# Optimization experiments

Hardware: AMD Instinct MI355X
Metric: run time of the kernel (lower is better)

## Reference

```python
import jax, jax.numpy as jnp
import numpy as np

N_NODES = 100000
N_EDGES = 1000000
D_IN = 64
D_OUT = 64


def setup_inputs() -> dict:
    key = jax.random.key(0)
    k_x, k_e, k_wl, k_bl, k_wr = jax.random.split(key, 5)
    x = jax.random.normal(k_x, (N_NODES, D_IN), dtype=jnp.float32)
    edge_index = jax.random.randint(k_e, (2, N_EDGES), 0, N_NODES, dtype=jnp.int64)
    scale = 1.0 / np.sqrt(D_IN)
    # SAGEConv params: lin_l (neighbor path, with bias), lin_r (root/self path, no bias)
    W_l = jax.random.uniform(k_wl, (D_OUT, D_IN), dtype=jnp.float32, minval=-scale, maxval=scale)
    b_l = jax.random.uniform(k_bl, (D_OUT,), dtype=jnp.float32, minval=-scale, maxval=scale)
    W_r = jax.random.uniform(k_wr, (D_OUT, D_IN), dtype=jnp.float32, minval=-scale, maxval=scale)
    return {"x": x, "edge_index": edge_index, "W_l": W_l, "b_l": b_l, "W_r": W_r}


def reference(x, edge_index, W_l, b_l, W_r):
    # PyG SAGEConv with mean aggregation:
    #   out = lin_l(mean_{j in N(i)} x_j) + lin_r(x_i);  then ReLU (from GCN.forward)
    src = edge_index[0]  # message sources
    dst = edge_index[1]  # aggregation targets
    n = x.shape[0]
    msg = x[src]  # [E, D_IN] gather
    agg = jax.ops.segment_sum(msg, dst, num_segments=n)  # [N, D_IN]
    deg = jax.ops.segment_sum(jnp.ones((src.shape[0],), x.dtype), dst, num_segments=n)
    mean = agg / jnp.maximum(deg, 1.0)[:, None]  # isolated nodes -> 0
    out = mean @ W_l.T + b_l + x @ W_r.T
    return jax.nn.relu(out)
```

## Files before the change

kernel.cpp:

```cpp
#include <hip/hip_runtime.h>

#define N_NODES 100000
#define N_EDGES 1000000
#define D 64

#define NFINE 782
#define CAP2 1536
#define CHUNK 2048
#define EDGE_BLOCKS 489
#define CONV_BLOCKS 6250
#define CONS_BLOCKS 3128
#define STR 132
#define SCAP 512

typedef unsigned short u16;
typedef unsigned int u32;
using bf16x8 = __attribute__((ext_vector_type(8))) short;
using f32x4  = __attribute__((ext_vector_type(4))) float;

__device__ __forceinline__ u16 f2bf(float f) {
    u32 u = __float_as_uint(f);
    return (u16)((u + 0x7FFF + ((u >> 16) & 1)) >> 16);
}
__device__ __forceinline__ float bf2f(u16 v) {
    return __uint_as_float(((u32)v) << 16);
}

__global__ __launch_bounds__(256) void conv_zero_kernel(
    const float* __restrict__ x, u16* __restrict__ xb,
    int* __restrict__ cur2) {
    if (blockIdx.x == CONV_BLOCKS) {
        for (int j = threadIdx.x; j < NFINE; j += 256) cur2[j] = 0;
        return;
    }
    int i = blockIdx.x * 256 + threadIdx.x;
    float4 v = ((const float4*)x)[i];
    ((ushort4*)xb)[i] = make_ushort4(f2bf(v.x), f2bf(v.y), f2bf(v.z), f2bf(v.w));
}

__global__ __launch_bounds__(1024) void build4_kernel(
    const int* __restrict__ ei, int* __restrict__ cur2,
    u32* __restrict__ pairs2) {
    __shared__ u32 sorted[CHUNK];
    __shared__ u16 binof[CHUNK];
    __shared__ int hist[NFINE];
    __shared__ int off_l[NFINE];
    __shared__ int cur_l[NFINE];
    __shared__ int base_g[NFINE];
    __shared__ int wsum[16];

    int b = blockIdx.x;
    int t = threadIdx.x;
    int ln = t & 63;
    int wv = t >> 6;

    const u32* uu = (const u32*)ei;
    int f = 1;
    #pragma unroll
    for (int i = 1; i < 16; i += 2)
        if (uu[i] != 0u) f = 0;

    if (t < NFINE) hist[t] = 0;
    __syncthreads();

    int e0 = b * CHUNK;
    int e1 = min(e0 + CHUNK, N_EDGES);
    int ne = e1 - e0;

    const uint2* e64 = (const uint2*)ei;
    int srcv[2], dstv[2];
    #pragma unroll
    for (int i = 0; i < 2; i++) {
        int ee = e0 + t + i * 1024;
        bool ok = ee < e1;
        if (f) {
            uint2 sv = ok ? e64[ee] : make_uint2(0u, 0u);
            uint2 dv = ok ? e64[N_EDGES + ee] : make_uint2(0u, 0u);
            srcv[i] = (int)sv.x;
            dstv[i] = ok ? (int)dv.x : -1;
        } else {
            srcv[i] = ok ? ei[ee] : 0;
            dstv[i] = ok ? ei[N_EDGES + ee] : -1;
        }
    }
    #pragma unroll
    for (int i = 0; i < 2; i++)
        if (dstv[i] >= 0) atomicAdd(&hist[dstv[i] >> 7], 1);
    __syncthreads();

    int h = (t < NFINE) ? hist[t] : 0;
    int inc = h;
    #pragma unroll
    for (int o = 1; o < 64; o <<= 1) {
        int v = __shfl_up(inc, o);
        if (ln >= o) inc += v;
    }
    if (ln == 63) wsum[wv] = inc;
    __syncthreads();
    if (t < 16) {
        int w = wsum[t];
        int winc = w;
        #pragma unroll
        for (int o = 1; o < 16; o <<= 1) {
            int v = __shfl_up(winc, o);
            if (t >= o) winc += v;
        }
        wsum[t] = winc - w;
    }
    __syncthreads();
    if (t < NFINE) {
        int ex = inc - h + wsum[wv];
        off_l[t] = ex;
        cur_l[t] = ex;
        base_g[t] = h ? atomicAdd(&cur2[t], h) : 0;
    }
    __syncthreads();

    #pragma unroll
    for (int i = 0; i < 2; i++) {
        if (dstv[i] >= 0) {
            int fine = dstv[i] >> 7;
            int slot = atomicAdd(&cur_l[fine], 1);
            sorted[slot] = (u32)srcv[i] | ((u32)(dstv[i] & 127) << 17);
            binof[slot] = (u16)fine;
        }
    }
    __syncthreads();

    for (int i = t; i < ne; i += 1024) {
        int fine = binof[i];
        int pos = base_g[fine] + (i - off_l[fine]);
        if (pos < CAP2)
            pairs2[(size_t)fine * CAP2 + pos] = sorted[i];
    }
}

__global__ __launch_bounds__(256) void cons6_kernel(
    const u16* __restrict__ xb, const float* __restrict__ Wl,
    const float* __restrict__ bl, const float* __restrict__ Wr,
    const int* __restrict__ cur2, const u32* __restrict__ pairs2,
    float* __restrict__ out) {
    __shared__ u16 Bs[64 * STR];
    __shared__ u16 As[32 * STR];
    __shared__ int sorted_s[SCAP];
    __shared__ int deg_l[32];
    __shared__ int off_l[32];
    __shared__ int cur_l[32];

    int tid = threadIdx.x;
    int bin = blockIdx.x >> 2;
    int quarter = blockIdx.x & 3;
    int nbase = bin * 128 + quarter * 32;
    if (nbase >= N_NODES) return;

    int lane = tid & 63;
    int wv = tid >> 6;

    int cnt = min(cur2[bin], CAP2);
    const u32* pb = &pairs2[(size_t)bin * CAP2];
    u32 ve[6];
    #pragma unroll
    for (int i = 0; i < 6; i++) {
        int e = tid + i * 256;
        ve[i] = (e < cnt) ? pb[e] : 0xFFFFFFFFu;
    }

    if (tid < 32) { deg_l[tid] = 0; cur_l[tid] = 0; }
    if (tid == 0) sorted_s[0] = 0;

    {
        int row = tid >> 2;
        int seg = tid & 3;
        const float4* wlf = (const float4*)Wl;
        const float4* wrf = (const float4*)Wr;
        #pragma unroll
        for (int j = 0; j < 4; j++) {
            float4 a = wlf[row * 16 + seg * 4 + j];
            float4 bq = wrf[row * 16 + seg * 4 + j];
            *(ushort4*)&Bs[row * STR + seg * 16 + j * 4] =
                make_ushort4(f2bf(a.x), f2bf(a.y), f2bf(a.z), f2bf(a.w));
            *(ushort4*)&Bs[row * STR + 64 + seg * 16 + j * 4] =
                make_ushort4(f2bf(bq.x), f2bf(bq.y), f2bf(bq.z), f2bf(bq.w));
        }
    }
    __syncthreads();

    #pragma unroll
    for (int i = 0; i < 6; i++) {
        u32 v = ve[i];
        if ((int)(v >> 22) == quarter) atomicAdd(&deg_l[(v >> 17) & 31], 1);
    }
    __syncthreads();

    if (tid < 32) {
        int dd = deg_l[tid];
        int inc = dd;
        #pragma unroll
        for (int o = 1; o < 32; o <<= 1) {
            int v = __shfl_up(inc, o);
            if (tid >= o) inc += v;
        }
        off_l[tid] = inc - dd;
    }
    __syncthreads();

    #pragma unroll
    for (int i = 0; i < 6; i++) {
        u32 v = ve[i];
        if ((int)(v >> 22) == quarter) {
            int lnn = (v >> 17) & 31;
            int p = off_l[lnn] + atomicAdd(&cur_l[lnn], 1);
            if (p < SCAP) sorted_s[p] = (int)(v & 0x1FFFFu);
        }
    }
    __syncthreads();

    int nl8 = lane >> 3;
    int c = lane & 7;
    int nl = wv * 8 + nl8;
    int n = nbase + nl;
    int d = deg_l[nl];
    int st = off_l[nl];

    int maxd = d;
    maxd = max(maxd, __shfl_xor(maxd, 8));
    maxd = max(maxd, __shfl_xor(maxd, 16));
    maxd = max(maxd, __shfl_xor(maxd, 32));

    float acc[8];
    #pragma unroll
    for (int j = 0; j < 8; j++) acc[j] = 0.0f;

    int dm1 = (d > 0) ? (d - 1) : 0;
    int sb = (d > 0) ? st : 0;
    for (int k = 0; k < maxd; k += 4) {
        int i0 = sb + min(k + 0, dm1);
        int i1 = sb + min(k + 1, dm1);
        int i2 = sb + min(k + 2, dm1);
        int i3 = sb + min(k + 3, dm1);
        int s0 = sorted_s[i0];
        int s1 = sorted_s[i1];
        int s2 = sorted_s[i2];
        int s3 = sorted_s[i3];
        bf16x8 r0 = *(const bf16x8*)&xb[(size_t)s0 * D + c * 8];
        bf16x8 r1 = *(const bf16x8*)&xb[(size_t)s1 * D + c * 8];
        bf16x8 r2 = *(const bf16x8*)&xb[(size_t)s2 * D + c * 8];
        bf16x8 r3 = *(const bf16x8*)&xb[(size_t)s3 * D + c * 8];
        float m0 = (k + 0 < d) ? 1.0f : 0.0f;
        float m1 = (k + 1 < d) ? 1.0f : 0.0f;
        float m2 = (k + 2 < d) ? 1.0f : 0.0f;
        float m3 = (k + 3 < d) ? 1.0f : 0.0f;
        #pragma unroll
        for (int j = 0; j < 8; j++)
            acc[j] = fmaf(m0, bf2f((u16)r0[j]), acc[j]);
        #pragma unroll
        for (int j = 0; j < 8; j++)
            acc[j] = fmaf(m1, bf2f((u16)r1[j]), acc[j]);
        #pragma unroll
        for (int j = 0; j < 8; j++)
            acc[j] = fmaf(m2, bf2f((u16)r2[j]), acc[j]);
        #pragma unroll
        for (int j = 0; j < 8; j++)
            acc[j] = fmaf(m3, bf2f((u16)r3[j]), acc[j]);
    }

    float inv = (d > 0) ? (1.0f / (float)d) : 0.0f;
    bf16x8 p;
    #pragma unroll
    for (int j = 0; j < 8; j++) p[j] = (short)f2bf(acc[j] * inv);
    *(bf16x8*)&As[nl * STR + c * 8] = p;
    bf16x8 xr = {0, 0, 0, 0, 0, 0, 0, 0};
    if (n < N_NODES) xr = *(const bf16x8*)&xb[(size_t)n * D + c * 8];
    *(bf16x8*)&As[nl * STR + 64 + c * 8] = xr;
    __syncthreads();

    int mtile = wv >> 1;
    int nt0 = (wv & 1) * 2;
    int lrow = lane & 15;
    int quad = lane >> 4;

    const u16* Ab  = &As[(mtile * 16 + lrow) * STR + quad * 8];
    const u16* Bb0 = &Bs[((nt0 + 0) * 16 + lrow) * STR + quad * 8];
    const u16* Bb1 = &Bs[((nt0 + 1) * 16 + lrow) * STR + quad * 8];

    float bias0 = bl[(nt0 + 0) * 16 + lrow];
    float bias1 = bl[(nt0 + 1) * 16 + lrow];
    f32x4 acc0 = {bias0, bias0, bias0, bias0};
    f32x4 acc1 = {bias1, bias1, bias1, bias1};

    #pragma unroll
    for (int kk = 0; kk < 4; kk++) {
        bf16x8 af = *(const bf16x8*)&Ab[kk * 32];
        bf16x8 b0 = *(const bf16x8*)&Bb0[kk * 32];
        bf16x8 b1 = *(const bf16x8*)&Bb1[kk * 32];
        acc0 = __builtin_amdgcn_mfma_f32_16x16x32_bf16(af, b0, acc0, 0, 0, 0);
        acc1 = __builtin_amdgcn_mfma_f32_16x16x32_bf16(af, b1, acc1, 0, 0, 0);
    }

    int node = nbase + mtile * 16 + quad * 4;
    #pragma unroll
    for (int r = 0; r < 4; r++) {
        if (node + r < N_NODES) {
            out[(size_t)(node + r) * D + (nt0 + 0) * 16 + lrow] = fmaxf(acc0[r], 0.0f);
            out[(size_t)(node + r) * D + (nt0 + 1) * 16 + lrow] = fmaxf(acc1[r], 0.0f);
        }
    }
}

extern "C" void kernel_launch(void* const* d_in, const int* in_sizes, int n_in,
                              void* d_out, int out_size, void* d_ws, size_t ws_size,
                              hipStream_t stream) {
    const float* x  = (const float*)d_in[0];
    const int*   ei = (const int*)d_in[1];
    const float* Wl = (const float*)d_in[2];
    const float* bl = (const float*)d_in[3];
    const float* Wr = (const float*)d_in[4];
    float* out = (float*)d_out;

    char* p = (char*)d_ws;
    int* cur2   = (int*)p;                        p += 1024 * sizeof(int);
    u32* pairs2 = (u32*)p;                        p += (size_t)NFINE * CAP2 * sizeof(u32);
    u16* xb     = (u16*)p;

    conv_zero_kernel<<<CONV_BLOCKS + 1, 256, 0, stream>>>(x, xb, cur2);
    build4_kernel<<<EDGE_BLOCKS, 1024, 0, stream>>>(ei, cur2, pairs2);
    cons6_kernel<<<CONS_BLOCKS, 256, 0, stream>>>(xb, Wl, bl, Wr, cur2, pairs2, out);
}
```

Measured before the change: 142.8 us.

## Pre-convert weights to bf16 once, double edge chunk, unroll gather by 8

Weight fp32-to-bf16 conversion moves out of every consumer block into one extra block of the conversion kernel, writing a shared bf16 weight buffer. The consumer kernel then loads its MFMA B fragments straight from global memory into registers and drops the weight staging in LDS, cutting per-block work and LDS use. The edge-bucketing kernel processes 4096 edges per block with half as many blocks, and the neighbor gather loop is unrolled to 8 loads per step for more memory-level parallelism. The costs are higher register pressure and fewer build blocks, which may lower occupancy or parallelism.

```diff
diff --git a/kernel.cpp b/kernel.cpp
--- a/kernel.cpp
+++ b/kernel.cpp
@@ -6,8 +6,8 @@
 
 #define NFINE 782
 #define CAP2 1536
-#define CHUNK 2048
-#define EDGE_BLOCKS 489
+#define CHUNK 4096
+#define EDGE_BLOCKS 245
 #define CONV_BLOCKS 6250
 #define CONS_BLOCKS 3128
 #define STR 132
@@ -28,17 +28,34 @@
 
 __global__ __launch_bounds__(256) void conv_zero_kernel(
     const float* __restrict__ x, u16* __restrict__ xb,
-    int* __restrict__ cur2) {
+    int* __restrict__ cur2,
+    const float* __restrict__ Wl, const float* __restrict__ Wr,
+    u16* __restrict__ Wb) {
     if (blockIdx.x == CONV_BLOCKS) {
         for (int j = threadIdx.x; j < NFINE; j += 256) cur2[j] = 0;
         return;
     }
+    if (blockIdx.x == CONV_BLOCKS + 1) {
+        int o = threadIdx.x >> 2;
+        int k0 = (threadIdx.x & 3) * 32;
+        const float4* wlf = (const float4*)Wl;
+        const float4* wrf = (const float4*)Wr;
+        #pragma unroll
+        for (int j = 0; j < 8; j++) {
+            int k = k0 + j * 4;
+            float4 v = (k < 64) ? wlf[(o * 64 + k) >> 2]
+                                : wrf[(o * 64 + k - 64) >> 2];
+            *(ushort4*)&Wb[o * 128 + k] =
+                make_ushort4(f2bf(v.x), f2bf(v.y), f2bf(v.z), f2bf(v.w));
+        }
+        return;
+    }
     int i = blockIdx.x * 256 + threadIdx.x;
     float4 v = ((const float4*)x)[i];
     ((ushort4*)xb)[i] = make_ushort4(f2bf(v.x), f2bf(v.y), f2bf(v.z), f2bf(v.w));
 }
 
-__global__ __launch_bounds__(1024) void build4_kernel(
+__global__ __launch_bounds__(1024) void build3_kernel(
     const int* __restrict__ ei, int* __restrict__ cur2,
     u32* __restrict__ pairs2) {
     __shared__ u32 sorted[CHUNK];
@@ -68,9 +85,9 @@
     int ne = e1 - e0;
 
     const uint2* e64 = (const uint2*)ei;
-    int srcv[2], dstv[2];
-    #pragma unroll
-    for (int i = 0; i < 2; i++) {
+    int srcv[4], dstv[4];
+    #pragma unroll
+    for (int i = 0; i < 4; i++) {
         int ee = e0 + t + i * 1024;
         bool ok = ee < e1;
         if (f) {
@@ -84,7 +101,7 @@
         }
     }
     #pragma unroll
-    for (int i = 0; i < 2; i++)
+    for (int i = 0; i < 4; i++)
         if (dstv[i] >= 0) atomicAdd(&hist[dstv[i] >> 7], 1);
     __syncthreads();
 
@@ -117,7 +134,7 @@
     __syncthreads();
 
     #pragma unroll
-    for (int i = 0; i < 2; i++) {
+    for (int i = 0; i < 4; i++) {
         if (dstv[i] >= 0) {
             int fine = dstv[i] >> 7;
             int slot = atomicAdd(&cur_l[fine], 1);
@@ -135,12 +152,11 @@
     }
 }
 
-__global__ __launch_bounds__(256) void cons6_kernel(
-    const u16* __restrict__ xb, const float* __restrict__ Wl,
-    const float* __restrict__ bl, const float* __restrict__ Wr,
+__global__ __launch_bounds__(256) void cons7_kernel(
+    const u16* __restrict__ xb, const u16* __restrict__ Wb,
+    const float* __restrict__ bl,
     const int* __restrict__ cur2, const u32* __restrict__ pairs2,
     float* __restrict__ out) {
-    __shared__ u16 Bs[64 * STR];
     __shared__ u16 As[32 * STR];
     __shared__ int sorted_s[SCAP];
     __shared__ int deg_l[32];
@@ -167,22 +183,6 @@
 
     if (tid < 32) { deg_l[tid] = 0; cur_l[tid] = 0; }
     if (tid == 0) sorted_s[0] = 0;
-
-    {
-        int row = tid >> 2;
-        int seg = tid & 3;
-        const float4* wlf = (const float4*)Wl;
-        const float4* wrf = (const float4*)Wr;
-        #pragma unroll
-        for (int j = 0; j < 4; j++) {
-            float4 a = wlf[row * 16 + seg * 4 + j];
-            float4 bq = wrf[row * 16 + seg * 4 + j];
-            *(ushort4*)&Bs[row * STR + seg * 16 + j * 4] =
-                make_ushort4(f2bf(a.x), f2bf(a.y), f2bf(a.z), f2bf(a.w));
-            *(ushort4*)&Bs[row * STR + 64 + seg * 16 + j * 4] =
-                make_ushort4(f2bf(bq.x), f2bf(bq.y), f2bf(bq.z), f2bf(bq.w));
-        }
-    }
     __syncthreads();
 
     #pragma unroll
@@ -233,36 +233,67 @@
 
     int dm1 = (d > 0) ? (d - 1) : 0;
     int sb = (d > 0) ? st : 0;
-    for (int k = 0; k < maxd; k += 4) {
-        int i0 = sb + min(k + 0, dm1);
-        int i1 = sb + min(k + 1, dm1);
-        int i2 = sb + min(k + 2, dm1);
-        int i3 = sb + min(k + 3, dm1);
-        int s0 = sorted_s[i0];
-        int s1 = sorted_s[i1];
-        int s2 = sorted_s[i2];
-        int s3 = sorted_s[i3];
+    for (int k = 0; k < maxd; k += 8) {
+        int ix[8];
+        #pragma unroll
+        for (int u = 0; u < 8; u++) ix[u] = sb + min(k + u, dm1);
+        int s0 = sorted_s[ix[0]];
+        int s1 = sorted_s[ix[1]];
+        int s2 = sorted_s[ix[2]];
+        int s3 = sorted_s[ix[3]];
+        int s4 = sorted_s[ix[4]];
+        int s5 = sorted_s[ix[5]];
+        int s6 = sorted_s[ix[6]];
+        int s7 = sorted_s[ix[7]];
         bf16x8 r0 = *(const bf16x8*)&xb[(size_t)s0 * D + c * 8];
         bf16x8 r1 = *(const bf16x8*)&xb[(size_t)s1 * D + c * 8];
         bf16x8 r2 = *(const bf16x8*)&xb[(size_t)s2 * D + c * 8];
         bf16x8 r3 = *(const bf16x8*)&xb[(size_t)s3 * D + c * 8];
+        bf16x8 r4 = *(const bf16x8*)&xb[(size_t)s4 * D + c * 8];
+        bf16x8 r5 = *(const bf16x8*)&xb[(size_t)s5 * D + c * 8];
+        bf16x8 r6 = *(const bf16x8*)&xb[(size_t)s6 * D + c * 8];
+        bf16x8 r7 = *(const bf16x8*)&xb[(size_t)s7 * D + c * 8];
         float m0 = (k + 0 < d) ? 1.0f : 0.0f;
         float m1 = (k + 1 < d) ? 1.0f : 0.0f;
         float m2 = (k + 2 < d) ? 1.0f : 0.0f;
         float m3 = (k + 3 < d) ? 1.0f : 0.0f;
-        #pragma unroll
-        for (int j = 0; j < 8; j++)
-            acc[j] = fmaf(m0, bf2f((u16)r0[j]), acc[j]);
-        #pragma unroll
-        for (int j = 0; j < 8; j++)
-            acc[j] = fmaf(m1, bf2f((u16)r1[j]), acc[j]);
-        #pragma unroll
-        for (int j = 0; j < 8; j++)
-            acc[j] = fmaf(m2, bf2f((u16)r2[j]), acc[j]);
-        #pragma unroll
-        for (int j = 0; j < 8; j++)
-            acc[j] = fmaf(m3, bf2f((u16)r3[j]), acc[j]);
-    }
+        float m4 = (k + 4 < d) ? 1.0f : 0.0f;
+        float m5 = (k + 5 < d) ? 1.0f : 0.0f;
+        float m6 = (k + 6 < d) ? 1.0f : 0.0f;
+        float m7 = (k + 7 < d) ? 1.0f : 0.0f;
+        #pragma unroll
+        for (int j = 0; j < 8; j++) acc[j] = fmaf(m0, bf2f((u16)r0[j]), acc[j]);
+        #pragma unroll
+        for (int j = 0; j < 8; j++) acc[j] = fmaf(m1, bf2f((u16)r1[j]), acc[j]);
+        #pragma unroll
+        for (int j = 0; j < 8; j++) acc[j] = fmaf(m2, bf2f((u16)r2[j]), acc[j]);
+        #pragma unroll
+        for (int j = 0; j < 8; j++) acc[j] = fmaf(m3, bf2f((u16)r3[j]), acc[j]);
+        #pragma unroll
+        for (int j = 0; j < 8; j++) acc[j] = fmaf(m4, bf2f((u16)r4[j]), acc[j]);
+        #pragma unroll
+        for (int j = 0; j < 8; j++) acc[j] = fmaf(m5, bf2f((u16)r5[j]), acc[j]);
+        #pragma unroll
+        for (int j = 0; j < 8; j++) acc[j] = fmaf(m6, bf2f((u16)r6[j]), acc[j]);
+        #pragma unroll
+        for (int j = 0; j < 8; j++) acc[j] = fmaf(m7, bf2f((u16)r7[j]), acc[j]);
+    }
+
+    int mtile = wv >> 1;
+    int nt0 = (wv & 1) * 2;
+    int lrow = lane & 15;
+    int quad = lane >> 4;
+
+    const u16* wb0 = &Wb[((nt0 + 0) * 16 + lrow) * 128 + quad * 8];
+    const u16* wb1 = &Wb[((nt0 + 1) * 16 + lrow) * 128 + quad * 8];
+    bf16x8 bf0_0 = *(const bf16x8*)&wb0[0 * 32];
+    bf16x8 bf0_1 = *(const bf16x8*)&wb0[1 * 32];
+    bf16x8 bf0_2 = *(const bf16x8*)&wb0[2 * 32];
+    bf16x8 bf0_3 = *(const bf16x8*)&wb0[3 * 32];
+    bf16x8 bf1_0 = *(const bf16x8*)&wb1[0 * 32];
+    bf16x8 bf1_1 = *(const bf16x8*)&wb1[1 * 32];
+    bf16x8 bf1_2 = *(const bf16x8*)&wb1[2 * 32];
+    bf16x8 bf1_3 = *(const bf16x8*)&wb1[3 * 32];
 
     float inv = (d > 0) ? (1.0f / (float)d) : 0.0f;
     bf16x8 p;
@@ -274,27 +305,27 @@
     *(bf16x8*)&As[nl * STR + 64 + c * 8] = xr;
     __syncthreads();
 
-    int mtile = wv >> 1;
-    int nt0 = (wv & 1) * 2;
-    int lrow = lane & 15;
-    int quad = lane >> 4;
-
-    const u16* Ab  = &As[(mtile * 16 + lrow) * STR + quad * 8];
-    const u16* Bb0 = &Bs[((nt0 + 0) * 16 + lrow) * STR + quad * 8];
-    const u16* Bb1 = &Bs[((nt0 + 1) * 16 + lrow) * STR + quad * 8];
+    const u16* Ab = &As[(mtile * 16 + lrow) * STR + quad * 8];
 
     float bias0 = bl[(nt0 + 0) * 16 + lrow];
     float bias1 = bl[(nt0 + 1) * 16 + lrow];
     f32x4 acc0 = {bias0, bias0, bias0, bias0};
     f32x4 acc1 = {bias1, bias1, bias1, bias1};
 
-    #pragma unroll
-    for (int kk = 0; kk < 4; kk++) {
-        bf16x8 af = *(const bf16x8*)&Ab[kk * 32];
-        bf16x8 b0 = *(const bf16x8*)&Bb0[kk * 32];
-        bf16x8 b1 = *(const bf16x8*)&Bb1[kk * 32];
-        acc0 = __builtin_amdgcn_mfma_f32_16x16x32_bf16(af, b0, acc0, 0, 0, 0);
-        acc1 = __builtin_amdgcn_mfma_f32_16x16x32_bf16(af, b1, acc1, 0, 0, 0);
+    {
+        bf16x8 af;
+        af = *(const bf16x8*)&Ab[0 * 32];
+        acc0 = __builtin_amdgcn_mfma_f32_16x16x32_bf16(af, bf0_0, acc0, 0, 0, 0);
+        acc1 = __builtin_amdgcn_mfma_f32_16x16x32_bf16(af, bf1_0, acc1, 0, 0, 0);
+        af = *(const bf16x8*)&Ab[1 * 32];
+        acc0 = __builtin_amdgcn_mfma_f32_16x16x32_bf16(af, bf0_1, acc0, 0, 0, 0);
+        acc1 = __builtin_amdgcn_mfma_f32_16x16x32_bf16(af, bf1_1, acc1, 0, 0, 0);
+        af = *(const bf16x8*)&Ab[2 * 32];
+        acc0 = __builtin_amdgcn_mfma_f32_16x16x32_bf16(af, bf0_2, acc0, 0, 0, 0);
+        acc1 = __builtin_amdgcn_mfma_f32_16x16x32_bf16(af, bf1_2, acc1, 0, 0, 0);
+        af = *(const bf16x8*)&Ab[3 * 32];
+        acc0 = __builtin_amdgcn_mfma_f32_16x16x32_bf16(af, bf0_3, acc0, 0, 0, 0);
+        acc1 = __builtin_amdgcn_mfma_f32_16x16x32_bf16(af, bf1_3, acc1, 0, 0, 0);
     }
 
     int node = nbase + mtile * 16 + quad * 4;
@@ -319,10 +350,11 @@
 
     char* p = (char*)d_ws;
     int* cur2   = (int*)p;                        p += 1024 * sizeof(int);
+    u16* Wb     = (u16*)p;                        p += 8192 * sizeof(u16);
     u32* pairs2 = (u32*)p;                        p += (size_t)NFINE * CAP2 * sizeof(u32);
     u16* xb     = (u16*)p;
 
-    conv_zero_kernel<<<CONV_BLOCKS + 1, 256, 0, stream>>>(x, xb, cur2);
-    build4_kernel<<<EDGE_BLOCKS, 1024, 0, stream>>>(ei, cur2, pairs2);
-    cons6_kernel<<<CONS_BLOCKS, 256, 0, stream>>>(xb, Wl, bl, Wr, cur2, pairs2, out);
-}
+    conv_zero_kernel<<<CONV_BLOCKS + 2, 256, 0, stream>>>(x, xb, cur2, Wl, Wr, Wb);
+    build3_kernel<<<EDGE_BLOCKS, 1024, 0, stream>>>(ei, cur2, pairs2);
+    cons7_kernel<<<CONS_BLOCKS, 256, 0, stream>>>(xb, Wb, bl, cur2, pairs2, out);
+}
```

Result: faster. 130.8 us (-8.4%).
